# Performance work log

Measured on AMD Instinct MI355X. Metric: run time of the kernel, lower is better.

Reference implementation:

```python
import jax, jax.numpy as jnp
import numpy as np

N, E, D, G, L = 100000, 3200000, 64, 64, 5
BN_EPS = 1e-5


def setup_inputs() -> dict:
    key = jax.random.key(0)
    ks = jax.random.split(key, 16)
    s = 0.05
    inp = {
        'x': jax.random.normal(ks[0], (N, D), jnp.float32),
        'edge_index': jax.random.randint(ks[1], (2, E), 0, N, dtype=jnp.int64),
        'edge_attr': jax.random.normal(ks[2], (E, 1), jnp.float32),
        'batch': jnp.sort(jax.random.randint(ks[3], (N,), 0, G, dtype=jnp.int64)),
        # per-layer GINEConv params (stacked over the 5 layers)
        'eps': jnp.zeros((L,), jnp.float32),                       # train_eps=True, init 0
        'edgeW': jax.random.normal(ks[4], (L, 1, D), jnp.float32) * s,  # Linear(edge_dim=1, D)
        'edgeB': jnp.zeros((L, D), jnp.float32),
        'W1': jax.random.normal(ks[5], (L, D, D), jnp.float32) * s,
        'b1': jnp.zeros((L, D), jnp.float32),
        'bn_g': jnp.ones((L, D), jnp.float32),                     # BatchNorm1d weight
        'bn_b': jnp.zeros((L, D), jnp.float32),                    # BatchNorm1d bias
        'W2': jax.random.normal(ks[6], (L, D, D), jnp.float32) * s,
        'b2': jnp.zeros((L, D), jnp.float32),
        'lin1W': jax.random.normal(ks[7], (5 * D, 4 * D), jnp.float32) * s,
        'lin1b': jnp.zeros((4 * D,), jnp.float32),
        'lin2W': jax.random.normal(ks[8], (4 * D, 5), jnp.float32) * s,
        'lin2b': jnp.zeros((5,), jnp.float32),
    }
    return inp


def reference(x, edge_index, edge_attr, batch, eps, edgeW, edgeB, W1, b1,
              bn_g, bn_b, W2, b2, lin1W, lin1b, lin2W, lin2b):
    src, dst = edge_index[0], edge_index[1]
    inv_std = 1.0 / jnp.sqrt(jnp.float32(1.0 + BN_EPS))  # BN eval mode: running_mean=0, running_var=1

    def gine_layer(h, i):
        e = edge_attr @ edgeW[i] + edgeB[i]                 # [E, D] edge embedding
        msg = jax.nn.relu(h[src] + e)                       # gather + add + relu
        aggr = jax.ops.segment_sum(msg, dst, num_segments=N)  # scatter-sum at target nodes
        z = (1.0 + eps[i]) * h + aggr
        z = z @ W1[i] + b1[i]
        z = z * (bn_g[i] * inv_std) + bn_b[i]               # BatchNorm1d (eval)
        z = jax.nn.relu(z)
        z = jax.nn.relu(z @ W2[i] + b2[i])
        return z

    hs = []
    h = x
    for i in range(L):
        h = gine_layer(h, i)
        hs.append(h)

    pooled = [jax.ops.segment_max(hk, batch, num_segments=G) for hk in hs]  # global_max_pool
    g = jnp.concatenate(pooled, axis=1)                     # [G, 5*D]
    g = jax.nn.relu(g @ lin1W + lin1b)
    # dropout p=0.5 is identity in eval mode
    out = g @ lin2W + lin2b                                 # [G, 5]
    return out
```

## Files before the change

kernel.cpp:

```cpp
#include <hip/hip_runtime.h>

#define N_NODES 100000
#define N_EDGES 3200000
#define D 64
#define G_GRAPHS 64
#define L_LAYERS 5
#define BN_EPS 1e-5f
#define RPW 8
#define NBUCK 196
#define BSHIFT 9
#define BMASK 511
#define NPB 512
#define EPB 6250
#define TOTC (NBUCK * NPB)
#define SCAN_CH 392

typedef __fp16 h2 __attribute__((ext_vector_type(2)));
union h2u { unsigned u; h2 h; };
typedef short v8s __attribute__((ext_vector_type(8)));
typedef float v4f __attribute__((ext_vector_type(4)));

__device__ __forceinline__ unsigned pkf16(float a, float b) {
    h2u x; x.h = __builtin_amdgcn_cvt_pkrtz(a, b); return x.u;
}

__device__ __forceinline__ unsigned short f2bf(float f) {
    unsigned int u = __float_as_uint(f);
    u += 0x7FFFu + ((u >> 16) & 1u);
    return (unsigned short)(u >> 16);
}
__device__ __forceinline__ float bf2f(unsigned short v) {
    return __uint_as_float((unsigned int)v << 16);
}

__device__ __forceinline__ void gload_lds16(const void* g, void* l) {
    __builtin_amdgcn_global_load_lds(
        (const __attribute__((address_space(1))) unsigned int*)g,
        (__attribute__((address_space(3))) unsigned int*)l, 16, 0, 0);
}

__device__ __forceinline__ unsigned quant15(float a) {
    float q = fminf(fmaxf((a + 8.0f) * 2048.0f, 0.0f), 32767.0f);
    return (unsigned)__float2int_rn(q);
}

__global__ __launch_bounds__(256) void xcvt_kernel(const float* __restrict__ x,
                                                   ushort* __restrict__ xbf) {
    const float4* x4 = (const float4*)x;
    ushort4* o4 = (ushort4*)xbf;
    const int total = N_NODES * D / 4;
    for (int i = blockIdx.x * blockDim.x + threadIdx.x; i < total;
         i += gridDim.x * blockDim.x) {
        float4 v = x4[i];
        ushort4 o;
        o.x = f2bf(v.x); o.y = f2bf(v.y); o.z = f2bf(v.z); o.w = f2bf(v.w);
        o4[i] = o;
    }
}

__global__ __launch_bounds__(256) void hist512_kernel(const int* __restrict__ ei,
                                                      int* __restrict__ gcount) {
    __shared__ int cnt[NBUCK];
    const int tid = threadIdx.x, b = blockIdx.x;
    if (tid < NBUCK) cnt[tid] = 0;
    __syncthreads();
    const int ebase = b * EPB, eend = ebase + EPB;
    for (int r = 0; r < 25; ++r) {
        int e = ebase + r * 256 + tid;
        if (e < eend) atomicAdd(&cnt[ei[N_EDGES + e] >> BSHIFT], 1);
    }
    __syncthreads();
    if (tid < NBUCK) gcount[tid * NPB + b] = cnt[tid];
}

__global__ __launch_bounds__(256) void scan_partial(const int* __restrict__ gcount,
                                                    int* __restrict__ bsum) {
    __shared__ int sc[256];
    int b = blockIdx.x, t = threadIdx.x;
    int s = b * SCAN_CH, e = min(s + SCAN_CH, TOTC);
    int sum = 0;
    for (int idx = s + t; idx < e; idx += 256) sum += gcount[idx];
    sc[t] = sum;
    __syncthreads();
    for (int o = 128; o; o >>= 1) {
        if (t < o) sc[t] += sc[t + o];
        __syncthreads();
    }
    if (!t) bsum[b] = sc[0];
}

__global__ __launch_bounds__(256) void scan_base(const int* __restrict__ bsum,
                                                 int* __restrict__ bbase,
                                                 int* __restrict__ bucketbase) {
    __shared__ int sc[256];
    int t = threadIdx.x;
    int v = bsum[t];
    sc[t] = v;
    __syncthreads();
    for (int o = 1; o < 256; o <<= 1) {
        int x = (t >= o) ? sc[t - o] : 0;
        __syncthreads();
        sc[t] += x;
        __syncthreads();
    }
    bbase[t] = sc[t] - v;
    if (t == 0) bucketbase[NBUCK] = N_EDGES;
}

__global__ __launch_bounds__(256) void scan_apply(const int* __restrict__ gcount,
                                                  const int* __restrict__ bbase,
                                                  int* __restrict__ ofs,
                                                  int* __restrict__ bucketbase) {
    __shared__ int sc[256];
    int b = blockIdx.x, t = threadIdx.x;
    int s = b * SCAN_CH, e = min(s + SCAN_CH, TOTC);
    int base = bbase[b];
    for (int t0 = s; t0 < e; t0 += 256) {
        int idx = t0 + t;
        int v = (idx < e) ? gcount[idx] : 0;
        sc[t] = v;
        __syncthreads();
        for (int o = 1; o < 256; o <<= 1) {
            int x = (t >= o) ? sc[t - o] : 0;
            __syncthreads();
            sc[t] += x;
            __syncthreads();
        }
        if (idx < e) {
            int ex = base + sc[t] - v;
            ofs[idx] = ex;
            if ((idx & (NPB - 1)) == 0) bucketbase[idx / NPB] = ex;
        }
        base += sc[255];
        __syncthreads();
    }
}

__global__ __launch_bounds__(256) void part_kernel(const int* __restrict__ ei,
                                                   const float* __restrict__ ea,
                                                   const int* __restrict__ ofs,
                                                   uint2* __restrict__ inter) {
    __shared__ int cur[NBUCK];
    const int tid = threadIdx.x, b = blockIdx.x;
    if (tid < NBUCK) cur[tid] = ofs[tid * NPB + b];
    __syncthreads();
    const int ebase = b * EPB, eend = ebase + EPB;
    for (int r = 0; r < 25; ++r) {
        int e = ebase + r * 256 + tid;
        if (e < eend) {
            int s = ei[e];
            int d = ei[N_EDGES + e];
            float a = ea[e];
            int k = d >> BSHIFT;
            int p = atomicAdd(&cur[k], 1);
            uint2 v;
            v.x = (unsigned)s;
            v.y = (unsigned)(d & BMASK) | (quant15(a) << BSHIFT);
            inter[p] = v;
        }
    }
}

__global__ __launch_bounds__(256) void bucket_kernel(const uint2* __restrict__ inter,
                                                     const int* __restrict__ bucketbase,
                                                     unsigned* __restrict__ perm,
                                                     int* __restrict__ row_ptr) {
    __shared__ int hist[512];
    __shared__ int part[256];
    const int b = blockIdx.x, t = threadIdx.x;
    const int beg = bucketbase[b], end = bucketbase[b + 1];
    const int cnt = end - beg;
    const uint2* reg = inter + beg;
    const int n0 = b << BSHIFT;
    const int nn = min(512, N_NODES - n0);
    hist[t] = 0; hist[t + 256] = 0;
    __syncthreads();
    for (int i = t; i < cnt; i += 256)
        atomicAdd(&hist[reg[i].y & BMASK], 1);
    __syncthreads();
    int h0 = hist[2 * t], h1 = hist[2 * t + 1];
    int s = h0 + h1;
    part[t] = s;
    __syncthreads();
    for (int o = 1; o < 256; o <<= 1) {
        int v = (t >= o) ? part[t - o] : 0;
        __syncthreads();
        part[t] += v;
        __syncthreads();
    }
    int ex = beg + part[t] - s;
    if (2 * t < nn)     row_ptr[n0 + 2 * t] = ex;
    if (2 * t + 1 < nn) row_ptr[n0 + 2 * t + 1] = ex + h0;
    hist[2 * t] = ex;
    hist[2 * t + 1] = ex + h0;
    __syncthreads();
    for (int i = t; i < cnt; i += 256) {
        uint2 v = reg[i];
        int p = atomicAdd(&hist[v.y & BMASK], 1);
        perm[p] = (v.x << 15) | (v.y >> BSHIFT);
    }
    if (b == NBUCK - 1 && t == 0) row_ptr[N_NODES] = N_EDGES;
}

__global__ __launch_bounds__(256, 3) void layer_kernel(
    const ushort* __restrict__ hbf,
    const int* __restrict__ row_ptr,
    const unsigned* __restrict__ perm,
    const float* __restrict__ eps, int layer,
    const float* __restrict__ edgeW, const float* __restrict__ edgeB,
    const float* __restrict__ W1, const float* __restrict__ b1,
    const float* __restrict__ bng, const float* __restrict__ bnb,
    const float* __restrict__ W2, const float* __restrict__ b2,
    const int* __restrict__ batch,
    ushort* __restrict__ hout,
    float* __restrict__ pooled ) {
    __shared__ ushort Wf1[4096];
    __shared__ ushort Wf2[4096];
    __shared__ __align__(16) ushort stage[4][3][1024];
    __shared__ __align__(16) ushort zbufs[4][512];
    __shared__ __align__(16) unsigned pbuf[4][512];

    const float inv_std = rsqrtf(1.0f + BN_EPS);
    const int tid = threadIdx.x;
    for (int idx = tid; idx < 4096; idx += 256) {
        int frag = idx >> 9;
        int l = (idx >> 3) & 63;
        int j = idx & 7;
        int kh = frag & 1, nt = frag >> 1;
        int k = kh * 32 + ((l >> 4) << 3) + j;
        int c = nt * 16 + (l & 15);
        Wf1[idx] = f2bf(W1[k * 64 + c] * (bng[c] * inv_std));
        Wf2[idx] = f2bf(W2[k * 64 + c]);
    }
    __syncthreads();

    const int lane = tid & 63;
    const int q = lane & 15;
    const int grp = lane >> 4;
    const int wid = tid >> 6;
    const int wv = blockIdx.x * 4 + wid;
    const int r0 = wv * RPW;
    if (r0 >= N_NODES) return;

    int rpv = 0;
    if (lane < 9) rpv = row_ptr[r0 + lane];
    int cval = __shfl(rpv, lane + 1) - rpv;
    int bval = 0;
    if (lane < RPW) bval = batch[r0 + lane];
    const int segbase = __shfl(rpv, 0);
    const int seglen  = __shfl(rpv, 8) - segbase;

    const float ev = 1.0f + eps[layer];
    const float QDEC = 4.8828125e-4f;
    float w4[4], b4[4];
    {
        float4 t = ((const float4*)edgeW)[q];
        w4[0] = t.x; w4[1] = t.y; w4[2] = t.z; w4[3] = t.w;
        float4 u = ((const float4*)edgeB)[q];
        b4[0] = u.x; b4[1] = u.y; b4[2] = u.z; b4[3] = u.w;
    }
    float blv1n[4], blv2n[4];
    #pragma unroll
    for (int nt = 0; nt < 4; ++nt) {
        int c = nt * 16 + (lane & 15);
        blv1n[nt] = fmaf(b1[c], bng[c] * inv_std, bnb[c]);
        blv2n[nt] = b2[c];
    }
    const ushort4* h4 = (const ushort4*)hbf;

    auto store_z = [&](int ai, float z0, float z1, float z2, float z3) {
        if (grp == 0) {
            unsigned lo = (unsigned)f2bf(z0) | ((unsigned)f2bf(z1) << 16);
            unsigned hi = (unsigned)f2bf(z2) | ((unsigned)f2bf(z3) << 16);
            int ad = (ai * 128 + q * 8) ^ ((ai & 7) << 4);
            *(uint2*)((char*)&zbufs[wid][0] + ad) = make_uint2(lo, hi);
        }
    };

    if (seglen <= 512) {
        if (seglen > 0) {
            gload_lds16(perm + segbase + lane * 4, &pbuf[wid][0]);
            if (seglen > 256)
                gload_lds16(perm + segbase + 256 + lane * 4, &pbuf[wid][256]);
        }
        asm volatile("s_waitcnt vmcnt(0)" ::: "memory");

        auto nchunks = [&](int i) { return (__shfl(cval, i) + 15) >> 4; };
        int nTot = 0;
        #pragma unroll
        for (int i = 0; i < RPW; ++i) nTot += nchunks(i);

        int i_iss = 0, c_iss = 0;
        while (i_iss < RPW && nchunks(i_iss) == 0) ++i_iss;
        auto issue1 = [&](int slot) {
            int rb = __shfl(rpv, i_iss) - segbase;
            int so = rb + (c_iss << 4);
            ushort* sb = &stage[wid][slot][0];
            int eloc = lane >> 3, sub = lane & 7;
            #pragma unroll
            for (int j = 0; j < 2; ++j) {
                int idx = min(so + (j << 3) + eloc, 511);
                unsigned pe = pbuf[wid][idx];
                gload_lds16(hbf + (size_t)(pe >> 15) * D + sub * 8, sb + j * 512);
            }
            ++c_iss;
            while (i_iss < RPW) {
                if (c_iss < nchunks(i_iss)) break;
                ++i_iss; c_iss = 0;
            }
        };
        auto accumulate = [&](const ushort* sb, int rb, int ebase, int cr, float* agg) {
            #pragma unroll
            for (int k = 0; k < 4; ++k) {
                int eidx = (k << 2) | grp;
                int idx = min(rb + ebase + eidx, 511);
                unsigned pe = pbuf[wid][idx];
                float m = (ebase + eidx < cr) ? 1.0f : 0.0f;
                float a = fmaf((float)(pe & 0x7FFFu), QDEC, -8.0f);
                ushort4 hv = *(const ushort4*)(sb + (eidx << 6) + (q << 2));
                agg[0] = fmaf(m, fmaxf(fmaf(a, w4[0], b4[0]) + bf2f(hv.x), 0.f), agg[0]);
                agg[1] = fmaf(m, fmaxf(fmaf(a, w4[1], b4[1]) + bf2f(hv.y), 0.f), agg[1]);
                agg[2] = fmaf(m, fmaxf(fmaf(a, w4[2], b4[2]) + bf2f(hv.z), 0.f), agg[2]);
                agg[3] = fmaf(m, fmaxf(fmaf(a, w4[3], b4[3]) + bf2f(hv.w), 0.f), agg[3]);
            }
        };

        int nIss = 0, sIss = 0, nCon = 0, sCon = 0;
        if (nIss < nTot) { issue1(sIss); sIss = 1; ++nIss; }
        if (nIss < nTot) { issue1(sIss); sIss = 2; ++nIss; }

        for (int ai = 0; ai < RPW; ++ai) {
            int cr = __shfl(cval, ai);
            int nch = (cr + 15) >> 4;
            int rb = __shfl(rpv, ai) - segbase;
            ushort4 hs4 = h4[(size_t)(r0 + ai) * 16 + q];
            float agg[4] = {0.f, 0.f, 0.f, 0.f};
            for (int ac = 0; ac < nch; ++ac) {
                if (nIss < nTot) {
                    issue1(sIss);
                    sIss = (sIss == 2) ? 0 : sIss + 1;
                    ++nIss;
                    asm volatile("s_waitcnt vmcnt(4)" ::: "memory");
                } else if (nIss - nCon == 2) {
                    asm volatile("s_waitcnt vmcnt(2)" ::: "memory");
                } else {
                    asm volatile("s_waitcnt vmcnt(0)" ::: "memory");
                }
                accumulate(&stage[wid][sCon][0], rb, ac << 4, cr, agg);
                sCon = (sCon == 2) ? 0 : sCon + 1;
                ++nCon;
            }
            #pragma unroll
            for (int c = 0; c < 4; ++c) {
                agg[c] += __shfl_xor(agg[c], 16);
                agg[c] += __shfl_xor(agg[c], 32);
            }
            store_z(ai,
                    fmaf(ev, bf2f(hs4.x), agg[0]), fmaf(ev, bf2f(hs4.y), agg[1]),
                    fmaf(ev, bf2f(hs4.z), agg[2]), fmaf(ev, bf2f(hs4.w), agg[3]));
        }
    } else {
        for (int ai = 0; ai < RPW; ++ai) {
            int cr = __shfl(cval, ai);
            int rbg = __shfl(rpv, ai);
            ushort4 hs4 = h4[(size_t)(r0 + ai) * 16 + q];
            float agg[4] = {0.f, 0.f, 0.f, 0.f};
            for (int k = grp; k < cr; k += 4) {
                unsigned pe = perm[rbg + k];
                float a = fmaf((float)(pe & 0x7FFFu), QDEC, -8.0f);
                ushort4 hv = h4[(size_t)(pe >> 15) * 16 + q];
                agg[0] += fmaxf(fmaf(a, w4[0], b4[0]) + bf2f(hv.x), 0.f);
                agg[1] += fmaxf(fmaf(a, w4[1], b4[1]) + bf2f(hv.y), 0.f);
                agg[2] += fmaxf(fmaf(a, w4[2], b4[2]) + bf2f(hv.z), 0.f);
                agg[3] += fmaxf(fmaf(a, w4[3], b4[3]) + bf2f(hv.w), 0.f);
            }
            #pragma unroll
            for (int c = 0; c < 4; ++c) {
                agg[c] += __shfl_xor(agg[c], 16);
                agg[c] += __shfl_xor(agg[c], 32);
            }
            store_z(ai,
                    fmaf(ev, bf2f(hs4.x), agg[0]), fmaf(ev, bf2f(hs4.y), agg[1]),
                    fmaf(ev, bf2f(hs4.z), agg[2]), fmaf(ev, bf2f(hs4.w), agg[3]));
        }
    }

    const int arow = lane & 15, agrp = lane >> 4;
    ushort* yb = &stage[wid][0][0];
    v8s a1[2];
    #pragma unroll
    for (int kh = 0; kh < 2; ++kh) {
        int ad = (arow * 128 + kh * 64 + agrp * 16) ^ ((arow & 7) << 4);
        a1[kh] = *(const v8s*)((char*)&zbufs[wid][0] + ad);
    }
    #pragma unroll
    for (int nt = 0; nt < 4; ++nt) {
        v4f acc = {0.f, 0.f, 0.f, 0.f};
        acc = __builtin_amdgcn_mfma_f32_16x16x32_bf16(
            a1[0], *(const v8s*)&Wf1[(nt * 2 + 0) * 512 + lane * 8], acc, 0, 0, 0);
        acc = __builtin_amdgcn_mfma_f32_16x16x32_bf16(
            a1[1], *(const v8s*)&Wf1[(nt * 2 + 1) * 512 + lane * 8], acc, 0, 0, 0);
        #pragma unroll
        for (int i = 0; i < 4; ++i) {
            float y = fmaxf(acc[i] + blv1n[nt], 0.f);
            int row = agrp * 4 + i;
            int ad = (row * 128 + (nt * 16 + arow) * 2) ^ ((row & 7) << 4);
            *(ushort*)((char*)yb + ad) = f2bf(y);
        }
    }
    v8s a2[2];
    #pragma unroll
    for (int kh = 0; kh < 2; ++kh) {
        int ad = (arow * 128 + kh * 64 + agrp * 16) ^ ((arow & 7) << 4);
        a2[kh] = *(const v8s*)((char*)yb + ad);
    }
    float y2v[16];
    #pragma unroll
    for (int nt = 0; nt < 4; ++nt) {
        v4f acc = {0.f, 0.f, 0.f, 0.f};
        acc = __builtin_amdgcn_mfma_f32_16x16x32_bf16(
            a2[0], *(const v8s*)&Wf2[(nt * 2 + 0) * 512 + lane * 8], acc, 0, 0, 0);
        acc = __builtin_amdgcn_mfma_f32_16x16x32_bf16(
            a2[1], *(const v8s*)&Wf2[(nt * 2 + 1) * 512 + lane * 8], acc, 0, 0, 0);
        #pragma unroll
        for (int i = 0; i < 4; ++i)
            y2v[nt * 4 + i] = fmaxf(acc[i] + blv2n[nt], 0.f);
    }
    if (agrp < 2) {
        #pragma unroll
        for (int i = 0; i < 4; ++i) {
            int row = agrp * 4 + i;
            #pragma unroll
            for (int nt = 0; nt < 4; ++nt)
                hout[(size_t)(r0 + row) * D + nt * 16 + arow] =
                    (ushort)f2bf(y2v[nt * 4 + i]);
        }
    }
    int g0 = __shfl(bval, 0), g7 = __shfl(bval, 7);
    if (g0 == g7) {
        #pragma unroll
        for (int nt = 0; nt < 4; ++nt) {
            float m = fmaxf(fmaxf(y2v[nt * 4 + 0], y2v[nt * 4 + 1]),
                            fmaxf(y2v[nt * 4 + 2], y2v[nt * 4 + 3]));
            m = fmaxf(m, __shfl_xor(m, 16));
            if (lane < 16)
                atomicMax((unsigned*)&pooled[g0 * D + nt * 16 + lane],
                          __float_as_uint(m));
        }
    } else {
        if (agrp < 2) {
            #pragma unroll
            for (int i = 0; i < 4; ++i) {
                int g = __shfl(bval, agrp * 4 + i);
                #pragma unroll
                for (int nt = 0; nt < 4; ++nt)
                    atomicMax((unsigned*)&pooled[g * D + nt * 16 + arow],
                              __float_as_uint(y2v[nt * 4 + i]));
            }
        }
    }
}

__global__ __launch_bounds__(256) void mlp_kernel(
    const float* __restrict__ pooled,
    const float* __restrict__ l1W, const float* __restrict__ l1b,
    const float* __restrict__ l2W, const float* __restrict__ l2b,
    float* __restrict__ out) {
    __shared__ float gl[5 * D];
    __shared__ float tl[4 * D];
    int gid = blockIdx.x;
    int tid = threadIdx.x;
    for (int idx = tid; idx < 5 * D; idx += 256) {
        int k = idx >> 6;
        int d = idx & 63;
        gl[idx] = pooled[k * (G_GRAPHS * D) + gid * D + d];
    }
    __syncthreads();
    {
        float acc = l1b[tid];
        for (int m = 0; m < 5 * D; ++m)
            acc = fmaf(gl[m], l1W[m * 256 + tid], acc);
        tl[tid] = fmaxf(acc, 0.0f);
    }
    __syncthreads();
    if (tid < 5) {
        float acc = l2b[tid];
        for (int m = 0; m < 4 * D; ++m)
            acc = fmaf(tl[m], l2W[m * 5 + tid], acc);
        out[gid * 5 + tid] = acc;
    }
}

extern "C" void kernel_launch(void* const* d_in, const int* in_sizes, int n_in,
                              void* d_out, int out_size, void* d_ws, size_t ws_size,
                              hipStream_t stream) {
    const float* x     = (const float*)d_in[0];
    const int*   ei    = (const int*)d_in[1];
    const float* ea    = (const float*)d_in[2];
    const int*   batch = (const int*)d_in[3];
    const float* eps   = (const float*)d_in[4];
    const float* edgeW = (const float*)d_in[5];
    const float* edgeB = (const float*)d_in[6];
    const float* W1    = (const float*)d_in[7];
    const float* b1    = (const float*)d_in[8];
    const float* bng   = (const float*)d_in[9];
    const float* bnb   = (const float*)d_in[10];
    const float* W2    = (const float*)d_in[11];
    const float* b2    = (const float*)d_in[12];
    const float* l1W   = (const float*)d_in[13];
    const float* l1b   = (const float*)d_in[14];
    const float* l2W   = (const float*)d_in[15];
    const float* l2b   = (const float*)d_in[16];
    float* out = (float*)d_out;

    char* ws = (char*)d_ws;
    size_t nbf = (size_t)N_NODES * D * sizeof(ushort);
    size_t off = 0;
    ushort* hbfA  = (ushort*)(ws + off); off += nbf;
    ushort* hbfB  = (ushort*)(ws + off); off += nbf;
    float* pooled = (float*)(ws + off);  off += (size_t)L_LAYERS * G_GRAPHS * D * sizeof(float);
    off = (off + 15) & ~(size_t)15;
    unsigned* perm = (unsigned*)(ws + off); off += (size_t)N_EDGES * sizeof(unsigned);
    int* row_ptr  = (int*)(ws + off);    off += (size_t)(N_NODES + 1) * sizeof(int);
    int* gcount   = (int*)(ws + off);    off += (size_t)TOTC * sizeof(int);
    int* ofs      = (int*)(ws + off);    off += (size_t)TOTC * sizeof(int);
    int* bucketbase = (int*)(ws + off);  off += (NBUCK + 4) * sizeof(int);
    int* bsum     = (int*)(ws + off);    off += 256 * sizeof(int);
    int* bbase    = (int*)(ws + off);    off += 256 * sizeof(int);
    off = (off + 15) & ~(size_t)15;
    uint2* inter  = (uint2*)(ws + off);  off += (size_t)N_EDGES * sizeof(uint2);

    hipMemsetAsync(pooled, 0, (size_t)L_LAYERS * G_GRAPHS * D * sizeof(float), stream);

    xcvt_kernel<<<1024, 256, 0, stream>>>(x, hbfA);
    hist512_kernel<<<NPB, 256, 0, stream>>>(ei, gcount);
    scan_partial<<<256, 256, 0, stream>>>(gcount, bsum);
    scan_base<<<1, 256, 0, stream>>>(bsum, bbase, bucketbase);
    scan_apply<<<256, 256, 0, stream>>>(gcount, bbase, ofs, bucketbase);
    part_kernel<<<NPB, 256, 0, stream>>>(ei, ea, ofs, inter);
    bucket_kernel<<<NBUCK, 256, 0, stream>>>(inter, bucketbase, perm, row_ptr);

    const int waves  = (N_NODES + RPW - 1) / RPW;
    const int blocks = (waves + 3) / 4;

    const ushort* hcur = hbfA;
    for (int i = 0; i < L_LAYERS; ++i) {
        ushort* hnext = (i & 1) ? hbfA : hbfB;
        layer_kernel<<<blocks, 256, 0, stream>>>(
            hcur, row_ptr, perm, eps, i,
            edgeW + i * D, edgeB + i * D,
            W1 + i * D * D, b1 + i * D,
            bng + i * D, bnb + i * D,
            W2 + i * D * D, b2 + i * D,
            batch, hnext, pooled + i * G_GRAPHS * D);
        hcur = hnext;
    }
    mlp_kernel<<<G_GRAPHS, 256, 0, stream>>>(pooled, l1W, l1b, l2W, l2b, out);
}
```

Baseline: 746.9 us.

## Switch node features to fp16 and aggregate edge messages with packed half math

Node features, weights and intermediates now use fp16 instead of bf16, and the MFMA calls move to the f16 variant. The edge-message inner loop now handles two edges at once with packed half add, fma and relu, then reduces into fp32 with fdot2 against a packed validity mask. This cuts VALU work per edge in the gather-aggregate phase. In exchange it adds fp16 range and precision risk in the message computation, and the edge-index buffer is padded and zero-filled so the clamping min() calls can be dropped.

```diff
diff --git a/kernel.cpp b/kernel.cpp
--- a/kernel.cpp
+++ b/kernel.cpp
@@ -17,21 +17,38 @@
 
 typedef __fp16 h2 __attribute__((ext_vector_type(2)));
 union h2u { unsigned u; h2 h; };
-typedef short v8s __attribute__((ext_vector_type(8)));
+typedef __fp16 v8h __attribute__((ext_vector_type(8)));
 typedef float v4f __attribute__((ext_vector_type(4)));
 
 __device__ __forceinline__ unsigned pkf16(float a, float b) {
     h2u x; x.h = __builtin_amdgcn_cvt_pkrtz(a, b); return x.u;
 }
-
-__device__ __forceinline__ unsigned short f2bf(float f) {
-    unsigned int u = __float_as_uint(f);
-    u += 0x7FFFu + ((u >> 16) & 1u);
-    return (unsigned short)(u >> 16);
-}
-__device__ __forceinline__ float bf2f(unsigned short v) {
-    return __uint_as_float((unsigned int)v << 16);
-}
+__device__ __forceinline__ float dot2(unsigned a, unsigned b, float c) {
+    h2u x, y; x.u = a; y.u = b;
+    return __builtin_amdgcn_fdot2(x.h, y.h, c, false);
+}
+__device__ __forceinline__ unsigned pk_add(unsigned a, unsigned b) {
+    h2u x, y, o; x.u = a; y.u = b; o.h = x.h + y.h; return o.u;
+}
+__device__ __forceinline__ unsigned pk_fma(unsigned a, unsigned b, unsigned c) {
+    h2u x, y, z, o; x.u = a; y.u = b; z.u = c;
+    o.h = x.h * y.h + z.h; return o.u;
+}
+__device__ __forceinline__ unsigned pk_relu(unsigned a) {
+    h2u x, z, o; x.u = a; z.u = 0;
+#if __has_builtin(__builtin_elementwise_max)
+    o.h = __builtin_elementwise_max(x.h, z.h);
+#else
+    o.h[0] = x.h[0] > (__fp16)0.f ? x.h[0] : (__fp16)0.f;
+    o.h[1] = x.h[1] > (__fp16)0.f ? x.h[1] : (__fp16)0.f;
+#endif
+    return o.u;
+}
+__device__ __forceinline__ ushort f2h(float f) {
+    union { __fp16 h; ushort s; } u; u.h = (__fp16)f; return u.s;
+}
+__device__ __forceinline__ float h2f_lo(unsigned v) { h2u u; u.u = v; return (float)u.h[0]; }
+__device__ __forceinline__ float h2f_hi(unsigned v) { h2u u; u.u = v; return (float)u.h[1]; }
 
 __device__ __forceinline__ void gload_lds16(const void* g, void* l) {
     __builtin_amdgcn_global_load_lds(
@@ -45,15 +62,15 @@
 }
 
 __global__ __launch_bounds__(256) void xcvt_kernel(const float* __restrict__ x,
-                                                   ushort* __restrict__ xbf) {
+                                                   ushort* __restrict__ xh) {
     const float4* x4 = (const float4*)x;
-    ushort4* o4 = (ushort4*)xbf;
+    ushort4* o4 = (ushort4*)xh;
     const int total = N_NODES * D / 4;
     for (int i = blockIdx.x * blockDim.x + threadIdx.x; i < total;
          i += gridDim.x * blockDim.x) {
         float4 v = x4[i];
         ushort4 o;
-        o.x = f2bf(v.x); o.y = f2bf(v.y); o.z = f2bf(v.z); o.w = f2bf(v.w);
+        o.x = f2h(v.x); o.y = f2h(v.y); o.z = f2h(v.z); o.w = f2h(v.w);
         o4[i] = o;
     }
 }
@@ -218,7 +235,7 @@
     __shared__ ushort Wf2[4096];
     __shared__ __align__(16) ushort stage[4][3][1024];
     __shared__ __align__(16) ushort zbufs[4][512];
-    __shared__ __align__(16) unsigned pbuf[4][512];
+    __shared__ __align__(16) unsigned pbuf[4][544];
 
     const float inv_std = rsqrtf(1.0f + BN_EPS);
     const int tid = threadIdx.x;
@@ -229,8 +246,8 @@
         int kh = frag & 1, nt = frag >> 1;
         int k = kh * 32 + ((l >> 4) << 3) + j;
         int c = nt * 16 + (l & 15);
-        Wf1[idx] = f2bf(W1[k * 64 + c] * (bng[c] * inv_std));
-        Wf2[idx] = f2bf(W2[k * 64 + c]);
+        Wf1[idx] = f2h(W1[k * 64 + c] * (bng[c] * inv_std));
+        Wf2[idx] = f2h(W2[k * 64 + c]);
     }
     __syncthreads();
 
@@ -253,11 +270,17 @@
     const float ev = 1.0f + eps[layer];
     const float QDEC = 4.8828125e-4f;
     float w4[4], b4[4];
+    unsigned wcc[4], bcc[4];
     {
         float4 t = ((const float4*)edgeW)[q];
         w4[0] = t.x; w4[1] = t.y; w4[2] = t.z; w4[3] = t.w;
         float4 u = ((const float4*)edgeB)[q];
         b4[0] = u.x; b4[1] = u.y; b4[2] = u.z; b4[3] = u.w;
+        #pragma unroll
+        for (int c = 0; c < 4; ++c) {
+            wcc[c] = pkf16(w4[c], w4[c]);
+            bcc[c] = pkf16(b4[c], b4[c]);
+        }
     }
     float blv1n[4], blv2n[4];
     #pragma unroll
@@ -266,12 +289,12 @@
         blv1n[nt] = fmaf(b1[c], bng[c] * inv_std, bnb[c]);
         blv2n[nt] = b2[c];
     }
-    const ushort4* h4 = (const ushort4*)hbf;
+    const uint2* h8 = (const uint2*)hbf;
 
     auto store_z = [&](int ai, float z0, float z1, float z2, float z3) {
         if (grp == 0) {
-            unsigned lo = (unsigned)f2bf(z0) | ((unsigned)f2bf(z1) << 16);
-            unsigned hi = (unsigned)f2bf(z2) | ((unsigned)f2bf(z3) << 16);
+            unsigned lo = pkf16(z0, z1);
+            unsigned hi = pkf16(z2, z3);
             int ad = (ai * 128 + q * 8) ^ ((ai & 7) << 4);
             *(uint2*)((char*)&zbufs[wid][0] + ad) = make_uint2(lo, hi);
         }
@@ -284,6 +307,7 @@
                 gload_lds16(perm + segbase + 256 + lane * 4, &pbuf[wid][256]);
         }
         asm volatile("s_waitcnt vmcnt(0)" ::: "memory");
+        for (int i = seglen + lane; i < 544; i += 64) pbuf[wid][i] = 0;
 
         auto nchunks = [&](int i) { return (__shfl(cval, i) + 15) >> 4; };
         int nTot = 0;
@@ -299,8 +323,7 @@
             int eloc = lane >> 3, sub = lane & 7;
             #pragma unroll
             for (int j = 0; j < 2; ++j) {
-                int idx = min(so + (j << 3) + eloc, 511);
-                unsigned pe = pbuf[wid][idx];
+                unsigned pe = pbuf[wid][so + (j << 3) + eloc];
                 gload_lds16(hbf + (size_t)(pe >> 15) * D + sub * 8, sb + j * 512);
             }
             ++c_iss;
@@ -311,17 +334,31 @@
         };
         auto accumulate = [&](const ushort* sb, int rb, int ebase, int cr, float* agg) {
             #pragma unroll
-            for (int k = 0; k < 4; ++k) {
-                int eidx = (k << 2) | grp;
-                int idx = min(rb + ebase + eidx, 511);
-                unsigned pe = pbuf[wid][idx];
-                float m = (ebase + eidx < cr) ? 1.0f : 0.0f;
-                float a = fmaf((float)(pe & 0x7FFFu), QDEC, -8.0f);
-                ushort4 hv = *(const ushort4*)(sb + (eidx << 6) + (q << 2));
-                agg[0] = fmaf(m, fmaxf(fmaf(a, w4[0], b4[0]) + bf2f(hv.x), 0.f), agg[0]);
-                agg[1] = fmaf(m, fmaxf(fmaf(a, w4[1], b4[1]) + bf2f(hv.y), 0.f), agg[1]);
-                agg[2] = fmaf(m, fmaxf(fmaf(a, w4[2], b4[2]) + bf2f(hv.z), 0.f), agg[2]);
-                agg[3] = fmaf(m, fmaxf(fmaf(a, w4[3], b4[3]) + bf2f(hv.w), 0.f), agg[3]);
+            for (int k = 0; k < 2; ++k) {
+                int e0 = (k << 3) | (grp << 1);
+                int base = rb + ebase + e0;
+                unsigned pe0 = pbuf[wid][base];
+                unsigned pe1 = pbuf[wid][base + 1];
+                int rem = cr - (ebase + e0);
+                unsigned mpk = (rem >= 2) ? 0x3C003C00u
+                             : ((rem == 1) ? 0x00003C00u : 0u);
+                float a0 = fmaf((float)(pe0 & 0x7FFFu), QDEC, -8.0f);
+                float a1 = fmaf((float)(pe1 & 0x7FFFu), QDEC, -8.0f);
+                unsigned apk = pkf16(a0, a1);
+                uint2 hv0 = *(const uint2*)(sb + (e0 << 6) + (q << 2));
+                uint2 hv1 = *(const uint2*)(sb + ((e0 + 1) << 6) + (q << 2));
+                unsigned p0 = __builtin_amdgcn_perm(hv1.x, hv0.x, 0x05040100u);
+                unsigned p1 = __builtin_amdgcn_perm(hv1.x, hv0.x, 0x07060302u);
+                unsigned p2 = __builtin_amdgcn_perm(hv1.y, hv0.y, 0x05040100u);
+                unsigned p3 = __builtin_amdgcn_perm(hv1.y, hv0.y, 0x07060302u);
+                unsigned m0 = pk_relu(pk_add(p0, pk_fma(apk, wcc[0], bcc[0])));
+                unsigned m1 = pk_relu(pk_add(p1, pk_fma(apk, wcc[1], bcc[1])));
+                unsigned m2 = pk_relu(pk_add(p2, pk_fma(apk, wcc[2], bcc[2])));
+                unsigned m3 = pk_relu(pk_add(p3, pk_fma(apk, wcc[3], bcc[3])));
+                agg[0] = dot2(m0, mpk, agg[0]);
+                agg[1] = dot2(m1, mpk, agg[1]);
+                agg[2] = dot2(m2, mpk, agg[2]);
+                agg[3] = dot2(m3, mpk, agg[3]);
             }
         };
 
@@ -333,7 +370,7 @@
             int cr = __shfl(cval, ai);
             int nch = (cr + 15) >> 4;
             int rb = __shfl(rpv, ai) - segbase;
-            ushort4 hs4 = h4[(size_t)(r0 + ai) * 16 + q];
+            uint2 hs = h8[(size_t)(r0 + ai) * 16 + q];
             float agg[4] = {0.f, 0.f, 0.f, 0.f};
             for (int ac = 0; ac < nch; ++ac) {
                 if (nIss < nTot) {
@@ -356,23 +393,23 @@
                 agg[c] += __shfl_xor(agg[c], 32);
             }
             store_z(ai,
-                    fmaf(ev, bf2f(hs4.x), agg[0]), fmaf(ev, bf2f(hs4.y), agg[1]),
-                    fmaf(ev, bf2f(hs4.z), agg[2]), fmaf(ev, bf2f(hs4.w), agg[3]));
+                    fmaf(ev, h2f_lo(hs.x), agg[0]), fmaf(ev, h2f_hi(hs.x), agg[1]),
+                    fmaf(ev, h2f_lo(hs.y), agg[2]), fmaf(ev, h2f_hi(hs.y), agg[3]));
         }
     } else {
         for (int ai = 0; ai < RPW; ++ai) {
             int cr = __shfl(cval, ai);
             int rbg = __shfl(rpv, ai);
-            ushort4 hs4 = h4[(size_t)(r0 + ai) * 16 + q];
+            uint2 hs = h8[(size_t)(r0 + ai) * 16 + q];
             float agg[4] = {0.f, 0.f, 0.f, 0.f};
             for (int k = grp; k < cr; k += 4) {
                 unsigned pe = perm[rbg + k];
                 float a = fmaf((float)(pe & 0x7FFFu), QDEC, -8.0f);
-                ushort4 hv = h4[(size_t)(pe >> 15) * 16 + q];
-                agg[0] += fmaxf(fmaf(a, w4[0], b4[0]) + bf2f(hv.x), 0.f);
-                agg[1] += fmaxf(fmaf(a, w4[1], b4[1]) + bf2f(hv.y), 0.f);
-                agg[2] += fmaxf(fmaf(a, w4[2], b4[2]) + bf2f(hv.z), 0.f);
-                agg[3] += fmaxf(fmaf(a, w4[3], b4[3]) + bf2f(hv.w), 0.f);
+                uint2 hv = h8[(size_t)(pe >> 15) * 16 + q];
+                agg[0] += fmaxf(fmaf(a, w4[0], b4[0]) + h2f_lo(hv.x), 0.f);
+                agg[1] += fmaxf(fmaf(a, w4[1], b4[1]) + h2f_hi(hv.x), 0.f);
+                agg[2] += fmaxf(fmaf(a, w4[2], b4[2]) + h2f_lo(hv.y), 0.f);
+                agg[3] += fmaxf(fmaf(a, w4[3], b4[3]) + h2f_hi(hv.y), 0.f);
             }
             #pragma unroll
             for (int c = 0; c < 4; ++c) {
@@ -380,48 +417,48 @@
                 agg[c] += __shfl_xor(agg[c], 32);
             }
             store_z(ai,
-                    fmaf(ev, bf2f(hs4.x), agg[0]), fmaf(ev, bf2f(hs4.y), agg[1]),
-                    fmaf(ev, bf2f(hs4.z), agg[2]), fmaf(ev, bf2f(hs4.w), agg[3]));
+                    fmaf(ev, h2f_lo(hs.x), agg[0]), fmaf(ev, h2f_hi(hs.x), agg[1]),
+                    fmaf(ev, h2f_lo(hs.y), agg[2]), fmaf(ev, h2f_hi(hs.y), agg[3]));
         }
     }
 
     const int arow = lane & 15, agrp = lane >> 4;
     ushort* yb = &stage[wid][0][0];
-    v8s a1[2];
+    v8h a1[2];
     #pragma unroll
     for (int kh = 0; kh < 2; ++kh) {
         int ad = (arow * 128 + kh * 64 + agrp * 16) ^ ((arow & 7) << 4);
-        a1[kh] = *(const v8s*)((char*)&zbufs[wid][0] + ad);
+        a1[kh] = *(const v8h*)((char*)&zbufs[wid][0] + ad);
     }
     #pragma unroll
     for (int nt = 0; nt < 4; ++nt) {
         v4f acc = {0.f, 0.f, 0.f, 0.f};
-        acc = __builtin_amdgcn_mfma_f32_16x16x32_bf16(
-            a1[0], *(const v8s*)&Wf1[(nt * 2 + 0) * 512 + lane * 8], acc, 0, 0, 0);
-        acc = __builtin_amdgcn_mfma_f32_16x16x32_bf16(
-            a1[1], *(const v8s*)&Wf1[(nt * 2 + 1) * 512 + lane * 8], acc, 0, 0, 0);
+        acc = __builtin_amdgcn_mfma_f32_16x16x32_f16(
+            a1[0], *(const v8h*)&Wf1[(nt * 2 + 0) * 512 + lane * 8], acc, 0, 0, 0);
+        acc = __builtin_amdgcn_mfma_f32_16x16x32_f16(
+            a1[1], *(const v8h*)&Wf1[(nt * 2 + 1) * 512 + lane * 8], acc, 0, 0, 0);
         #pragma unroll
         for (int i = 0; i < 4; ++i) {
             float y = fmaxf(acc[i] + blv1n[nt], 0.f);
             int row = agrp * 4 + i;
             int ad = (row * 128 + (nt * 16 + arow) * 2) ^ ((row & 7) << 4);
-            *(ushort*)((char*)yb + ad) = f2bf(y);
-        }
-    }
-    v8s a2[2];
+            *(ushort*)((char*)yb + ad) = f2h(y);
+        }
+    }
+    v8h a2[2];
     #pragma unroll
     for (int kh = 0; kh < 2; ++kh) {
         int ad = (arow * 128 + kh * 64 + agrp * 16) ^ ((arow & 7) << 4);
-        a2[kh] = *(const v8s*)((char*)yb + ad);
+        a2[kh] = *(const v8h*)((char*)yb + ad);
     }
     float y2v[16];
     #pragma unroll
     for (int nt = 0; nt < 4; ++nt) {
         v4f acc = {0.f, 0.f, 0.f, 0.f};
-        acc = __builtin_amdgcn_mfma_f32_16x16x32_bf16(
-            a2[0], *(const v8s*)&Wf2[(nt * 2 + 0) * 512 + lane * 8], acc, 0, 0, 0);
-        acc = __builtin_amdgcn_mfma_f32_16x16x32_bf16(
-            a2[1], *(const v8s*)&Wf2[(nt * 2 + 1) * 512 + lane * 8], acc, 0, 0, 0);
+        acc = __builtin_amdgcn_mfma_f32_16x16x32_f16(
+            a2[0], *(const v8h*)&Wf2[(nt * 2 + 0) * 512 + lane * 8], acc, 0, 0, 0);
+        acc = __builtin_amdgcn_mfma_f32_16x16x32_f16(
+            a2[1], *(const v8h*)&Wf2[(nt * 2 + 1) * 512 + lane * 8], acc, 0, 0, 0);
         #pragma unroll
         for (int i = 0; i < 4; ++i)
             y2v[nt * 4 + i] = fmaxf(acc[i] + blv2n[nt], 0.f);
@@ -433,7 +470,7 @@
             #pragma unroll
             for (int nt = 0; nt < 4; ++nt)
                 hout[(size_t)(r0 + row) * D + nt * 16 + arow] =
-                    (ushort)f2bf(y2v[nt * 4 + i]);
+                    f2h(y2v[nt * 4 + i]);
         }
     }
     int g0 = __shfl(bval, 0), g7 = __shfl(bval, 7);
```

New measurement: 833.5 us. 1.12x slower.
